# Optimization experiments

Hardware: AMD Instinct MI355X
Metric: run time of the kernel (lower is better)

## Reference

```python
import jax, jax.numpy as jnp
import numpy as np

N = 50000        # nodes
E = 800000       # edges
MUL = 32         # multiplicity per irrep (32x0e + 32x1o)
NSPEC = 4        # atom species (node_attrs one-hot width)
NBESSEL = 8      # edge_embedding basis size
HID = 8          # invariant_neurons
WNUM = 4 * MUL   # tp.weight_numel (4 'uvu' paths x 32)


def setup_inputs() -> dict:
    key = jax.random.key(0)
    ks = jax.random.split(key, 13)
    return {
        "edge_embedding": jax.random.normal(ks[0], (E, NBESSEL), jnp.float32),
        "node_attrs": jax.random.uniform(ks[1], (N, NSPEC), jnp.float32),
        "node_features": jax.random.normal(ks[2], (N, MUL * 4), jnp.float32),
        "edge_index": jax.random.randint(ks[3], (2, E), 0, N, jnp.int64),
        "edge_attrs": jax.random.normal(ks[4], (E, 4), jnp.float32),
        # linear_1 (per-irrep channel mixing)
        "W1_s": jax.random.normal(ks[5], (MUL, MUL), jnp.float32),
        "W1_v": jax.random.normal(ks[6], (MUL, MUL), jnp.float32),
        # fc: [8] -> [8] -> [128]
        "Wfc1": jax.random.normal(ks[7], (NBESSEL, HID), jnp.float32),
        "Wfc2": jax.random.normal(ks[8], (HID, WNUM), jnp.float32),
        # linear_2: 64x0e+64x1o -> 32x0e+32x1o
        "W2_s": jax.random.normal(ks[9], (2 * MUL, MUL), jnp.float32),
        "W2_v": jax.random.normal(ks[10], (2 * MUL, MUL), jnp.float32),
        # sc: FullyConnectedTensorProduct(32x0e+32x1o, 4x0e -> 32x0e+32x1o)
        "Wsc_s": jax.random.normal(ks[11], (MUL, NSPEC, MUL), jnp.float32),
        "Wsc_v": jax.random.normal(ks[12], (MUL, NSPEC, MUL), jnp.float32),
    }


def reference(edge_embedding, node_attrs, node_features, edge_index, edge_attrs,
              W1_s, W1_v, Wfc1, Wfc2, W2_s, W2_v, Wsc_s, Wsc_v):
    s = node_features[:, :MUL]                       # [N,32] 0e
    v = node_features[:, MUL:].reshape(N, MUL, 3)    # [N,32,3] 1o

    # self-connection: FullyConnectedTensorProduct(features, node_attrs)
    inv = 1.0 / np.sqrt(MUL * NSPEC).astype(np.float32)
    sc_s = jnp.einsum('nu,nz,uzv->nv', s, node_attrs, Wsc_s) * inv
    sc_v = jnp.einsum('nui,nz,uzv->nvi', v, node_attrs, Wsc_v) * inv

    # linear_1 (equivariant: mixes channels within each irrep)
    lin = np.float32(1.0 / np.sqrt(MUL))
    s1 = (s @ W1_s) * lin
    v1 = jnp.einsum('nui,uv->nvi', v, W1_v) * lin

    # fc MLP on edge_embedding -> per-edge TP weights [E,128]
    h = jax.nn.silu((edge_embedding @ Wfc1) * np.float32(1.0 / np.sqrt(NBESSEL)))
    w = (h @ Wfc2) * np.float32(1.0 / np.sqrt(HID))
    w0, w1, w2, w3 = w[:, :MUL], w[:, MUL:2*MUL], w[:, 2*MUL:3*MUL], w[:, 3*MUL:]

    ctr, nbr = edge_index[0], edge_index[1]
    xs = s1[nbr]            # [E,32] gathered scalars
    xv = v1[nbr]            # [E,32,3] gathered vectors
    es = edge_attrs[:, :1]  # [E,1]  edge 0e
    ev = edge_attrs[:, 1:4] # [E,3]  edge 1o

    # weighted CG tensor product ('uvu', per-edge weights)
    out_s0 = w0 * xs * es                                              # 0e x 0e -> 0e
    out_s3 = w3 * jnp.einsum('eui,ei->eu', xv, ev) * np.float32(1/np.sqrt(3))  # 1o x 1o -> 0e
    out_v1 = (w1 * xs)[:, :, None] * ev[:, None, :]                    # 0e x 1o -> 1o
    out_v2 = (w2 * es)[:, :, None] * xv                                # 1o x 0e -> 1o

    e_s = jnp.concatenate([out_s0, out_s3], axis=1)    # [E,64]
    e_v = jnp.concatenate([out_v1, out_v2], axis=1)    # [E,64,3]

    # scatter-sum back to center nodes
    n_s = jax.ops.segment_sum(e_s, ctr, num_segments=N)
    n_v = jax.ops.segment_sum(e_v.reshape(E, -1), ctr, num_segments=N).reshape(N, 2*MUL, 3)

    # linear_2 + residual self-connection
    lin2 = np.float32(1.0 / np.sqrt(2 * MUL))
    out_s = (n_s @ W2_s) * lin2 + sc_s
    out_v = jnp.einsum('nui,uv->nvi', n_v, W2_v) * lin2 + sc_v

    return jnp.concatenate([out_s, out_v.reshape(N, MUL * 3)], axis=1)
```

## Files before the change

kernel.cpp:

```cpp
#include <hip/hip_runtime.h>

#define N_NODES 50000
#define E_EDGES 800000
#define MUL 32
#define CAP 48

__device__ __forceinline__ unsigned bfpack2(float a, float b) {
    unsigned ua = __float_as_uint(a), ub = __float_as_uint(b);
    ua = (ua + 0x7FFFu + ((ua >> 16) & 1u)) >> 16;
    ub = (ub + 0x7FFFu + ((ub >> 16) & 1u)) >> 16;
    return ua | (ub << 16);
}
__device__ __forceinline__ float bflo(unsigned p) { return __uint_as_float(p << 16); }
__device__ __forceinline__ float bfhi(unsigned p) { return __uint_as_float(p & 0xFFFF0000u); }

__global__ __launch_bounds__(512) void node_pre_sc(
    const float* __restrict__ nf, const float* __restrict__ attrs,
    const float* __restrict__ W1s, const float* __restrict__ W1v,
    const float* __restrict__ Wscs, const float* __restrict__ Wscv,
    uint2* __restrict__ xq, float* __restrict__ out, int* __restrict__ cnt)
{
    for (int i = blockIdx.x * 512 + threadIdx.x; i < N_NODES; i += gridDim.x * 512)
        cnt[i] = 0;

    __shared__ float sW1s[1024];
    __shared__ float sW1v[1024];
    __shared__ float sWscsT[4096];
    __shared__ float sWscvT[4096];
    __shared__ float snf[16][128];
    __shared__ float sat[16][4];
    for (int i = threadIdx.x; i < 1024; i += 512) { sW1s[i] = W1s[i]; sW1v[i] = W1v[i]; }
    for (int i = threadIdx.x; i < 4096; i += 512) {
        int u = i >> 7, rem = i & 127, z = rem >> 5, vv = rem & 31;
        int t = ((u * 32 + vv) << 2) + z;
        sWscsT[t] = Wscs[i];
        sWscvT[t] = Wscv[i];
    }
    int g = threadIdx.x >> 5, v = threadIdx.x & 31;
    const float lin = 0.17677669529663687f;
    const float inv = 0.08838834764831845f;
    for (int node0 = blockIdx.x * 16; node0 < N_NODES; node0 += gridDim.x * 16) {
        __syncthreads();
        for (int i = threadIdx.x; i < 16 * 128; i += 512) {
            int nn = node0 + (i >> 7);
            snf[i >> 7][i & 127] = (nn < N_NODES) ? nf[(long long)nn * 128 + (i & 127)] : 0.f;
        }
        if (threadIdx.x < 64) {
            int nn = node0 + (threadIdx.x >> 2);
            sat[threadIdx.x >> 2][threadIdx.x & 3] = (nn < N_NODES) ? attrs[nn * 4 + (threadIdx.x & 3)] : 0.f;
        }
        __syncthreads();
        int n = node0 + g;
        if (n >= N_NODES) continue;
        float az0 = sat[g][0], az1 = sat[g][1], az2 = sat[g][2], az3 = sat[g][3];
        float acc_s = 0.f, a0 = 0.f, a1 = 0.f, a2 = 0.f;
        float scs = 0.f, scv0 = 0.f, scv1 = 0.f, scv2 = 0.f;
#pragma unroll
        for (int u = 0; u < 32; ++u) {
            float su = snf[g][u];
            float x0 = snf[g][32 + u * 3 + 0];
            float x1 = snf[g][32 + u * 3 + 1];
            float x2 = snf[g][32 + u * 3 + 2];
            acc_s += su * sW1s[u * 32 + v];
            float wv = sW1v[u * 32 + v];
            a0 += x0 * wv; a1 += x1 * wv; a2 += x2 * wv;
            int t = (u * 32 + v) << 2;
            float4 cs4 = *(const float4*)&sWscsT[t];
            float4 cv4 = *(const float4*)&sWscvT[t];
            float cs = az0 * cs4.x + az1 * cs4.y + az2 * cs4.z + az3 * cs4.w;
            scs += su * cs;
            float cv = az0 * cv4.x + az1 * cv4.y + az2 * cv4.z + az3 * cv4.w;
            scv0 += x0 * cv; scv1 += x1 * cv; scv2 += x2 * cv;
        }
        uint2 q;
        q.x = bfpack2(acc_s * lin, a0 * lin);
        q.y = bfpack2(a1 * lin, a2 * lin);
        xq[n * 32 + v] = q;
        long long ob = (long long)n * 128;
        out[ob + v] = scs * inv;
        out[ob + 32 + v * 3 + 0] = scv0 * inv;
        out[ob + 32 + v * 3 + 1] = scv1 * inv;
        out[ob + 32 + v * 3 + 2] = scv2 * inv;
    }
}

__global__ __launch_bounds__(256) void edge_prep(
    const float* __restrict__ ee, const float* __restrict__ Wfc1,
    const int* __restrict__ ei, const float* __restrict__ ea,
    int* __restrict__ cnt, int* __restrict__ nbrl, uint4* __restrict__ rec)
{
    __shared__ float sW[64];
    if (threadIdx.x < 64) sW[threadIdx.x] = Wfc1[threadIdx.x];
    __syncthreads();
    long long e = (long long)blockIdx.x * 256 + threadIdx.x;
    if (e >= E_EDGES) return;

    int c = ei[e];
    int nbr = ei[E_EDGES + e];
    int slot = atomicAdd(&cnt[c], 1);

    const float4* p = (const float4*)(ee + e * 8);
    float4 a = p[0], b = p[1];
    float emb[8] = {a.x, a.y, a.z, a.w, b.x, b.y, b.z, b.w};
    const float sfc = 0.35355339059327373f;
    float h[8];
#pragma unroll
    for (int k = 0; k < 8; ++k) {
        float acc = 0.f;
#pragma unroll
        for (int t = 0; t < 8; ++t) acc += emb[t] * sW[t * 8 + k];
        acc *= sfc;
        h[k] = acc / (1.f + __expf(-acc));
    }
    float4 av = ((const float4*)ea)[e];

    if (slot < CAP) {
        int idx = c * CAP + slot;
        nbrl[idx] = nbr;
        uint4 A;
        A.x = bfpack2(h[0], h[1]); A.y = bfpack2(h[2], h[3]);
        A.z = bfpack2(h[4], h[5]); A.w = bfpack2(h[6], h[7]);
        uint2 C;
        C.x = bfpack2(av.x, av.y); C.y = bfpack2(av.z, av.w);
        rec[(long long)idx * 2] = A;
        *(uint2*)(rec + (long long)idx * 2 + 1) = C;
    }
}

__global__ __launch_bounds__(256, 6) void gather(
    const int* __restrict__ cnt, const int* __restrict__ nbrl,
    const uint4* __restrict__ rec,
    const uint2* __restrict__ xq, const float* __restrict__ Wfc2,
    float4* __restrict__ m4)
{
    int wid = threadIdx.x >> 6;
    int lane = threadIdx.x & 63;
    int u = lane & 31;
    int half = lane >> 5;
    const float sfc = 0.35355339059327373f;
    const float is3 = 0.5773502691896258f;
    float wf0[8], wf1[8], wf2[8], wf3[8];
#pragma unroll
    for (int t = 0; t < 8; ++t) {
        wf0[t] = Wfc2[t * 128 + u] * sfc;
        wf1[t] = Wfc2[t * 128 + 32 + u] * sfc;
        wf2[t] = Wfc2[t * 128 + 64 + u] * sfc;
        wf3[t] = Wfc2[t * 128 + 96 + u] * sfc;
    }
    for (int n = blockIdx.x * 4 + wid; n < N_NODES; n += gridDim.x * 4) {
        int deg = cnt[n];
        if (deg > CAP) deg = CAP;
        int T = (deg + 1) >> 1;
        long long base = (long long)n * CAP;
        int nbr_all = (lane < deg) ? nbrl[base + lane] : 0;
        float as0 = 0.f, as3 = 0.f;
        float av10 = 0.f, av11 = 0.f, av12 = 0.f;
        float av20 = 0.f, av21 = 0.f, av22 = 0.f;
        uint4 A_c = {0, 0, 0, 0};
        uint2 C_c = {0, 0}, q_c = {0, 0};
        float m_c = 0.f;
        if (T > 0) {
            int j = half;
            m_c = (j < deg) ? 1.f : 0.f;
            int js = (j < deg) ? j : 0;
            int nbr = __shfl(nbr_all, js);
            A_c = rec[(base + js) * 2];
            C_c = *(const uint2*)(rec + (base + js) * 2 + 1);
            q_c = xq[nbr * 32 + u];
        }
        for (int t = 0; t < T; ++t) {
            uint4 A_n = {0, 0, 0, 0};
            uint2 C_n = {0, 0}, q_n = {0, 0};
            float m_n = 0.f;
            if (t + 1 < T) {
                int j = 2 * (t + 1) + half;
                m_n = (j < deg) ? 1.f : 0.f;
                int js = (j < deg) ? j : 0;
                int nbr = __shfl(nbr_all, js);
                A_n = rec[(base + js) * 2];
                C_n = *(const uint2*)(rec + (base + js) * 2 + 1);
                q_n = xq[nbr * 32 + u];
            }
            float hh[8] = {bflo(A_c.x), bfhi(A_c.x), bflo(A_c.y), bfhi(A_c.y),
                           bflo(A_c.z), bfhi(A_c.z), bflo(A_c.w), bfhi(A_c.w)};
            float w0 = 0.f, w1 = 0.f, w2 = 0.f, w3 = 0.f;
#pragma unroll
            for (int t8 = 0; t8 < 8; ++t8) {
                float ht = hh[t8];
                w0 += ht * wf0[t8];
                w1 += ht * wf1[t8];
                w2 += ht * wf2[t8];
                w3 += ht * wf3[t8];
            }
            w0 *= m_c; w1 *= m_c; w2 *= m_c; w3 *= m_c;
            float es  = bflo(C_c.x), ev0 = bfhi(C_c.x);
            float ev1 = bflo(C_c.y), ev2 = bfhi(C_c.y);
            float xs  = bflo(q_c.x), xv0 = bfhi(q_c.x);
            float xv1 = bflo(q_c.y), xv2 = bfhi(q_c.y);
            as0 += w0 * xs * es;
            as3 += w3 * (xv0 * ev0 + xv1 * ev1 + xv2 * ev2);
            float t1 = w1 * xs;
            float t2 = w2 * es;
            av10 += t1 * ev0; av11 += t1 * ev1; av12 += t1 * ev2;
            av20 += t2 * xv0; av21 += t2 * xv1; av22 += t2 * xv2;
            A_c = A_n; C_c = C_n; q_c = q_n; m_c = m_n;
        }
        as0  += __shfl_xor(as0, 32);
        as3  += __shfl_xor(as3, 32);
        av10 += __shfl_xor(av10, 32);
        av11 += __shfl_xor(av11, 32);
        av12 += __shfl_xor(av12, 32);
        av20 += __shfl_xor(av20, 32);
        av21 += __shfl_xor(av21, 32);
        av22 += __shfl_xor(av22, 32);
        if (half == 0) m4[(long long)n * 64 + u]      = make_float4(av10, av11, av12, as0);
        else           m4[(long long)n * 64 + 32 + u] = make_float4(av20, av21, av22, as3 * is3);
    }
}

__global__ __launch_bounds__(512) void node_post(
    const float4* __restrict__ m4,
    const float* __restrict__ W2s, const float* __restrict__ W2v,
    float* __restrict__ out)
{
    __shared__ float sW2s[2048];
    __shared__ float sW2v[2048];
    __shared__ float4 sm[16][64];
    for (int i = threadIdx.x; i < 2048; i += 512) { sW2s[i] = W2s[i]; sW2v[i] = W2v[i]; }
    int g = threadIdx.x >> 5, v = threadIdx.x & 31;
    const float lin2 = 0.125f;
    for (int node0 = blockIdx.x * 16; node0 < N_NODES; node0 += gridDim.x * 16) {
        __syncthreads();
        for (int i = threadIdx.x; i < 16 * 64; i += 512) {
            int nn = node0 + (i >> 6);
            sm[i >> 6][i & 63] = (nn < N_NODES) ? m4[(long long)nn * 64 + (i & 63)]
                                                : make_float4(0.f, 0.f, 0.f, 0.f);
        }
        __syncthreads();
        int n = node0 + g;
        if (n >= N_NODES) continue;
        float os = 0.f, ov0 = 0.f, ov1 = 0.f, ov2 = 0.f;
#pragma unroll 16
        for (int U = 0; U < 64; ++U) {
            float4 q = sm[g][U];
            os += q.w * sW2s[U * 32 + v];
            float wv = sW2v[U * 32 + v];
            ov0 += q.x * wv; ov1 += q.y * wv; ov2 += q.z * wv;
        }
        long long ob = (long long)n * 128;
        out[ob + v] += os * lin2;
        out[ob + 32 + v * 3 + 0] += ov0 * lin2;
        out[ob + 32 + v * 3 + 1] += ov1 * lin2;
        out[ob + 32 + v * 3 + 2] += ov2 * lin2;
    }
}

extern "C" void kernel_launch(void* const* d_in, const int* in_sizes, int n_in,
                              void* d_out, int out_size, void* d_ws, size_t ws_size,
                              hipStream_t stream) {
    const float* ee    = (const float*)d_in[0];
    const float* attrs = (const float*)d_in[1];
    const float* nf    = (const float*)d_in[2];
    const int*   ei    = (const int*)d_in[3];
    const float* ea    = (const float*)d_in[4];
    const float* W1s   = (const float*)d_in[5];
    const float* W1v   = (const float*)d_in[6];
    const float* Wfc1  = (const float*)d_in[7];
    const float* Wfc2  = (const float*)d_in[8];
    const float* W2s   = (const float*)d_in[9];
    const float* W2v   = (const float*)d_in[10];
    const float* Wscs  = (const float*)d_in[11];
    const float* Wscv  = (const float*)d_in[12];
    float* out = (float*)d_out;

    uint2*  xq   = (uint2*)d_ws;
    uint4*  rec  = (uint4*)(xq + (size_t)N_NODES * 32);
    float4* m4   = (float4*)(rec + (size_t)N_NODES * CAP * 2);
    int*    cnt  = (int*)(m4 + (size_t)N_NODES * 64);
    int*    nbrl = cnt + N_NODES;

    node_pre_sc<<<768, 512, 0, stream>>>(nf, attrs, W1s, W1v, Wscs, Wscv, xq, out, cnt);
    edge_prep<<<(E_EDGES + 255) / 256, 256, 0, stream>>>(ee, Wfc1, ei, ea, cnt, nbrl, rec);
    gather<<<2048, 256, 0, stream>>>(cnt, nbrl, rec, xq, Wfc2, m4);
    node_post<<<1024, 512, 0, stream>>>(m4, W2s, W2v, out);
}
```

Before: 394.2 us.

## Use fp16 packed dot products for edge weights; drop per-tile block barriers

```diff
diff --git a/kernel.cpp b/kernel.cpp
--- a/kernel.cpp
+++ b/kernel.cpp
@@ -4,6 +4,8 @@
 #define E_EDGES 800000
 #define MUL 32
 #define CAP 48
+
+typedef _Float16 half2v __attribute__((ext_vector_type(2)));
 
 __device__ __forceinline__ unsigned bfpack2(float a, float b) {
     unsigned ua = __float_as_uint(a), ub = __float_as_uint(b);
@@ -13,6 +15,13 @@
 }
 __device__ __forceinline__ float bflo(unsigned p) { return __uint_as_float(p << 16); }
 __device__ __forceinline__ float bfhi(unsigned p) { return __uint_as_float(p & 0xFFFF0000u); }
+__device__ __forceinline__ unsigned pkh2(float a, float b) {
+    union { _Float16 h[2]; unsigned u; } x;
+    x.h[0] = (_Float16)a; x.h[1] = (_Float16)b; return x.u;
+}
+__device__ __forceinline__ half2v ashalf2(unsigned u) {
+    union { unsigned u; half2v h; } x; x.u = u; return x.h;
+}
 
 __global__ __launch_bounds__(512) void node_pre_sc(
     const float* __restrict__ nf, const float* __restrict__ attrs,
@@ -28,7 +37,6 @@
     __shared__ float sWscsT[4096];
     __shared__ float sWscvT[4096];
     __shared__ float snf[16][128];
-    __shared__ float sat[16][4];
     for (int i = threadIdx.x; i < 1024; i += 512) { sW1s[i] = W1s[i]; sW1v[i] = W1v[i]; }
     for (int i = threadIdx.x; i < 4096; i += 512) {
         int u = i >> 7, rem = i & 127, z = rem >> 5, vv = rem & 31;
@@ -36,23 +44,25 @@
         sWscsT[t] = Wscs[i];
         sWscvT[t] = Wscv[i];
     }
+    __syncthreads();
     int g = threadIdx.x >> 5, v = threadIdx.x & 31;
+    int lane = threadIdx.x & 63;
+    int wbase = (threadIdx.x >> 6) * 2;
+    int sg = wbase + (lane >> 5);
     const float lin = 0.17677669529663687f;
     const float inv = 0.08838834764831845f;
+    const float4* nf4 = (const float4*)nf;
+    const float4* at4 = (const float4*)attrs;
     for (int node0 = blockIdx.x * 16; node0 < N_NODES; node0 += gridDim.x * 16) {
-        __syncthreads();
-        for (int i = threadIdx.x; i < 16 * 128; i += 512) {
-            int nn = node0 + (i >> 7);
-            snf[i >> 7][i & 127] = (nn < N_NODES) ? nf[(long long)nn * 128 + (i & 127)] : 0.f;
-        }
-        if (threadIdx.x < 64) {
-            int nn = node0 + (threadIdx.x >> 2);
-            sat[threadIdx.x >> 2][threadIdx.x & 3] = (nn < N_NODES) ? attrs[nn * 4 + (threadIdx.x & 3)] : 0.f;
-        }
-        __syncthreads();
+        {
+            int nn = node0 + sg;
+            float4 ld = (nn < N_NODES) ? nf4[(long long)nn * 32 + (lane & 31)]
+                                       : make_float4(0.f, 0.f, 0.f, 0.f);
+            *(float4*)&snf[sg][(lane & 31) * 4] = ld;
+        }
         int n = node0 + g;
         if (n >= N_NODES) continue;
-        float az0 = sat[g][0], az1 = sat[g][1], az2 = sat[g][2], az3 = sat[g][3];
+        float4 az = at4[n];
         float acc_s = 0.f, a0 = 0.f, a1 = 0.f, a2 = 0.f;
         float scs = 0.f, scv0 = 0.f, scv1 = 0.f, scv2 = 0.f;
 #pragma unroll
@@ -67,9 +77,9 @@
             int t = (u * 32 + v) << 2;
             float4 cs4 = *(const float4*)&sWscsT[t];
             float4 cv4 = *(const float4*)&sWscvT[t];
-            float cs = az0 * cs4.x + az1 * cs4.y + az2 * cs4.z + az3 * cs4.w;
+            float cs = az.x * cs4.x + az.y * cs4.y + az.z * cs4.z + az.w * cs4.w;
             scs += su * cs;
-            float cv = az0 * cv4.x + az1 * cv4.y + az2 * cv4.z + az3 * cv4.w;
+            float cv = az.x * cv4.x + az.y * cv4.y + az.z * cv4.z + az.w * cv4.w;
             scv0 += x0 * cv; scv1 += x1 * cv; scv2 += x2 * cv;
         }
         uint2 q;
@@ -118,8 +128,8 @@
         int idx = c * CAP + slot;
         nbrl[idx] = nbr;
         uint4 A;
-        A.x = bfpack2(h[0], h[1]); A.y = bfpack2(h[2], h[3]);
-        A.z = bfpack2(h[4], h[5]); A.w = bfpack2(h[6], h[7]);
+        A.x = pkh2(h[0], h[1]); A.y = pkh2(h[2], h[3]);
+        A.z = pkh2(h[4], h[5]); A.w = pkh2(h[6], h[7]);
         uint2 C;
         C.x = bfpack2(av.x, av.y); C.y = bfpack2(av.z, av.w);
         rec[(long long)idx * 2] = A;
@@ -139,13 +149,17 @@
     int half = lane >> 5;
     const float sfc = 0.35355339059327373f;
     const float is3 = 0.5773502691896258f;
-    float wf0[8], wf1[8], wf2[8], wf3[8];
+    half2v wf0[4], wf1[4], wf2[4], wf3[4];
 #pragma unroll
-    for (int t = 0; t < 8; ++t) {
-        wf0[t] = Wfc2[t * 128 + u] * sfc;
-        wf1[t] = Wfc2[t * 128 + 32 + u] * sfc;
-        wf2[t] = Wfc2[t * 128 + 64 + u] * sfc;
-        wf3[t] = Wfc2[t * 128 + 96 + u] * sfc;
+    for (int t = 0; t < 4; ++t) {
+        wf0[t] = half2v{(_Float16)(Wfc2[(2*t) * 128 + u] * sfc),
+                        (_Float16)(Wfc2[(2*t+1) * 128 + u] * sfc)};
+        wf1[t] = half2v{(_Float16)(Wfc2[(2*t) * 128 + 32 + u] * sfc),
+                        (_Float16)(Wfc2[(2*t+1) * 128 + 32 + u] * sfc)};
+        wf2[t] = half2v{(_Float16)(Wfc2[(2*t) * 128 + 64 + u] * sfc),
+                        (_Float16)(Wfc2[(2*t+1) * 128 + 64 + u] * sfc)};
+        wf3[t] = half2v{(_Float16)(Wfc2[(2*t) * 128 + 96 + u] * (sfc * is3)),
+                        (_Float16)(Wfc2[(2*t+1) * 128 + 96 + u] * (sfc * is3))};
     }
     for (int n = blockIdx.x * 4 + wid; n < N_NODES; n += gridDim.x * 4) {
         int deg = cnt[n];
@@ -181,17 +195,25 @@
                 C_n = *(const uint2*)(rec + (base + js) * 2 + 1);
                 q_n = xq[nbr * 32 + u];
             }
-            float hh[8] = {bflo(A_c.x), bfhi(A_c.x), bflo(A_c.y), bfhi(A_c.y),
-                           bflo(A_c.z), bfhi(A_c.z), bflo(A_c.w), bfhi(A_c.w)};
+            half2v h01 = ashalf2(A_c.x), h23 = ashalf2(A_c.y);
+            half2v h45 = ashalf2(A_c.z), h67 = ashalf2(A_c.w);
             float w0 = 0.f, w1 = 0.f, w2 = 0.f, w3 = 0.f;
-#pragma unroll
-            for (int t8 = 0; t8 < 8; ++t8) {
-                float ht = hh[t8];
-                w0 += ht * wf0[t8];
-                w1 += ht * wf1[t8];
-                w2 += ht * wf2[t8];
-                w3 += ht * wf3[t8];
-            }
+            w0 = __builtin_amdgcn_fdot2(h01, wf0[0], w0, false);
+            w1 = __builtin_amdgcn_fdot2(h01, wf1[0], w1, false);
+            w2 = __builtin_amdgcn_fdot2(h01, wf2[0], w2, false);
+            w3 = __builtin_amdgcn_fdot2(h01, wf3[0], w3, false);
+            w0 = __builtin_amdgcn_fdot2(h23, wf0[1], w0, false);
+            w1 = __builtin_amdgcn_fdot2(h23, wf1[1], w1, false);
+            w2 = __builtin_amdgcn_fdot2(h23, wf2[1], w2, false);
+            w3 = __builtin_amdgcn_fdot2(h23, wf3[1], w3, false);
+            w0 = __builtin_amdgcn_fdot2(h45, wf0[2], w0, false);
+            w1 = __builtin_amdgcn_fdot2(h45, wf1[2], w1, false);
+            w2 = __builtin_amdgcn_fdot2(h45, wf2[2], w2, false);
+            w3 = __builtin_amdgcn_fdot2(h45, wf3[2], w3, false);
+            w0 = __builtin_amdgcn_fdot2(h67, wf0[3], w0, false);
+            w1 = __builtin_amdgcn_fdot2(h67, wf1[3], w1, false);
+            w2 = __builtin_amdgcn_fdot2(h67, wf2[3], w2, false);
+            w3 = __builtin_amdgcn_fdot2(h67, wf3[3], w3, false);
             w0 *= m_c; w1 *= m_c; w2 *= m_c; w3 *= m_c;
             float es  = bflo(C_c.x), ev0 = bfhi(C_c.x);
             float ev1 = bflo(C_c.y), ev2 = bfhi(C_c.y);
@@ -214,7 +236,7 @@
         av21 += __shfl_xor(av21, 32);
         av22 += __shfl_xor(av22, 32);
         if (half == 0) m4[(long long)n * 64 + u]      = make_float4(av10, av11, av12, as0);
-        else           m4[(long long)n * 64 + 32 + u] = make_float4(av20, av21, av22, as3 * is3);
+        else           m4[(long long)n * 64 + 32 + u] = make_float4(av20, av21, av22, as3);
     }
 }
 
@@ -227,16 +249,21 @@
     __shared__ float sW2v[2048];
     __shared__ float4 sm[16][64];
     for (int i = threadIdx.x; i < 2048; i += 512) { sW2s[i] = W2s[i]; sW2v[i] = W2v[i]; }
+    __syncthreads();
     int g = threadIdx.x >> 5, v = threadIdx.x & 31;
+    int lane = threadIdx.x & 63;
+    int sg = (threadIdx.x >> 6) * 2 + (lane >> 5);
     const float lin2 = 0.125f;
     for (int node0 = blockIdx.x * 16; node0 < N_NODES; node0 += gridDim.x * 16) {
-        __syncthreads();
-        for (int i = threadIdx.x; i < 16 * 64; i += 512) {
-            int nn = node0 + (i >> 6);
-            sm[i >> 6][i & 63] = (nn < N_NODES) ? m4[(long long)nn * 64 + (i & 63)]
-                                                : make_float4(0.f, 0.f, 0.f, 0.f);
-        }
-        __syncthreads();
+        {
+            int nn = node0 + sg;
+            int s0 = (lane & 31) * 2;
+            float4 z = make_float4(0.f, 0.f, 0.f, 0.f);
+            float4 a = (nn < N_NODES) ? m4[(long long)nn * 64 + s0] : z;
+            float4 b = (nn < N_NODES) ? m4[(long long)nn * 64 + s0 + 1] : z;
+            sm[sg][s0] = a;
+            sm[sg][s0 + 1] = b;
+        }
         int n = node0 + g;
         if (n >= N_NODES) continue;
         float os = 0.f, ov0 = 0.f, ov1 = 0.f, ov2 = 0.f;
```

New measurement: 350.5 us. -11.1%, faster.
